# Kernel optimization log

Measured on AMD Instinct MI355X. Metric: run time of the kernel, lower is better.

The kernel has to match this reference:

```python
import jax, jax.numpy as jnp
import numpy as np

B, F_IN, N, S = 2, 128, 192, 192   # batch, in_features, n_nodes, seq (seq==n_nodes required by mask broadcast)
H, D = 4, 64                        # n_heads, n_hidden (out_features = H*D = 256)
NEG_SLOPE = 0.2


def setup_inputs() -> dict:
    key = jax.random.key(0)
    ks = jax.random.split(key, 6)
    X = jax.random.normal(ks[0], (B, F_IN, N, S), dtype=jnp.float32)
    A = jax.random.randint(ks[1], (N, N, 1), 0, 2, dtype=jnp.int32)
    W_lin = jax.random.normal(ks[2], (F_IN, H * D), dtype=jnp.float32) * 0.05
    b_lin = jax.random.uniform(ks[3], (H * D,), dtype=jnp.float32)
    W_attn = jax.random.normal(ks[4], (2 * D,), dtype=jnp.float32) * 0.05
    b_attn = jax.random.uniform(ks[5], (1,), dtype=jnp.float32)
    return {"X": X, "A": A, "W_lin": W_lin, "b_lin": b_lin,
            "W_attn": W_attn, "b_attn": b_attn}


def reference(X, A, W_lin, b_lin, W_attn, b_attn):
    # Dropout is identity (eval mode).
    b, f, n, s = X.shape
    x = jnp.transpose(X, (0, 3, 2, 1))                      # (b, s, n, f)
    g = (x @ W_lin + b_lin).reshape(b, s, n, H, D)          # (b, s, n, H, D)
    # attn is affine: attn(cat[g_i, g_j]) = a_src.g_i + a_dst.g_j + b_attn
    a_src, a_dst = W_attn[:D], W_attn[D:]
    s_src = jnp.einsum('bsnhd,d->bsnh', g, a_src)
    s_dst = jnp.einsum('bsnhd,d->bsnh', g, a_dst)
    e = s_src[:, :, :, None, :] + s_dst[:, :, None, :, :] + b_attn[0]  # (b, s, n_i, n_j, H)
    e = jnp.where(e >= 0, e, NEG_SLOPE * e)                 # LeakyReLU
    # torch masked_fill broadcast: mask (n,n,1,1) aligns with e dims (s, n_i, n_j, H)
    e = jnp.where(A[..., None] == 0, -jnp.inf, e)
    alphas = jax.nn.softmax(e, axis=1)                      # softmax over seq dim (dim=1, as in source)
    alphas = jnp.nan_to_num(alphas, nan=0.0)
    # einsum 'mnojh,klphf->mnohf': independent sums over j (alphas) and k,l,p (g)
    sum_g = g.sum(axis=(0, 1, 2))                           # (H, D)
    attn_res = alphas.sum(axis=3)[..., None] * sum_g        # (b, s, n, H, D)
    out = attn_res.reshape(b, s, n, H * D)                  # concat=True
    return jnp.transpose(out, (0, 3, 2, 1))                 # (b, out_features, n, s)
```

## Files before the change

kernel.cpp:

```cpp
#include <hip/hip_runtime.h>
#include <math.h>

#define B_ 2
#define F_ 128
#define N_ 192
#define S_ 192
#define NS_ (N_ * S_)
#define SLOPE 0.2f
#define LOG2E 1.4426950408889634f
#define NEG_INF (-__builtin_inff())

#if defined(__has_builtin)
#if __has_builtin(__builtin_amdgcn_exp2f)
#define EXP2(x) __builtin_amdgcn_exp2f(x)
#else
#define EXP2(x) exp2f(x)
#endif
#else
#define EXP2(x) exp2f(x)
#endif

__device__ __forceinline__ float lrelu(float e) { return fmaxf(e, SLOPE * e); }

#define OFF_WSRC 0
#define OFF_WDST 512
#define OFF_CSRC 1024
#define OFF_CDST 1028
#define OFF_SUMG 1040
#define OFF_PART 1296
#define OFF_SRC  2320
#define OFF_DST2 (OFF_SRC + 8 * NS_)
#define OFF_DST1 (OFF_DST2 + 8 * NS_)

__global__ __launch_bounds__(256) void kPre(const float* __restrict__ X,
                                            const float* __restrict__ W_lin,
                                            const float* __restrict__ b_lin,
                                            const float* __restrict__ W_attn,
                                            const float* __restrict__ b_attn,
                                            float* __restrict__ ws) {
    int blk = blockIdx.x, t = threadIdx.x;
    if (blk < 1024) {
        int sq = blk & 3, f = (blk >> 2) & 127, b = blk >> 9;
        const float4* p = (const float4*)(X + ((size_t)(b * F_ + f)) * NS_ + sq * 9216);
        float acc = 0.f;
#pragma unroll
        for (int k = 0; k < 9; k++) {
            float4 v = p[t + k * 256];
            acc += (v.x + v.y) + (v.z + v.w);
        }
        for (int o = 32; o; o >>= 1) acc += __shfl_down(acc, o, 64);
        __shared__ float red[4];
        if ((t & 63) == 0) red[t >> 6] = acc;
        __syncthreads();
        if (t == 0)
            ws[OFF_PART + sq * 256 + b * 128 + f] = (red[0] + red[1]) + (red[2] + red[3]);
    } else if (blk == 1024) {
        const float4* wa = (const float4*)W_attn;
        for (int c = t; c < 512; c += 256) {
            int f = c >> 2, h = c & 3;
            const float4* wl = (const float4*)(W_lin + f * 256 + h * 64);
            float as = 0.f, ad = 0.f;
#pragma unroll
            for (int q = 0; q < 16; q++) {
                float4 w = wl[q], a1 = wa[q], a2 = wa[16 + q];
                as += w.x * a1.x + w.y * a1.y + w.z * a1.z + w.w * a1.w;
                ad += w.x * a2.x + w.y * a2.y + w.z * a2.z + w.w * a2.w;
            }
            ws[OFF_WSRC + c] = as * LOG2E;
            ws[OFF_WDST + c] = ad * LOG2E;
        }
    } else {
        if (t < 4) {
            float c = 0.f;
            for (int d = 0; d < 64; d++) c += b_lin[t * 64 + d] * W_attn[d];
            ws[OFF_CSRC + t] = (c + b_attn[0]) * LOG2E;
        } else if (t < 8) {
            int h = t - 4;
            float c = 0.f;
            for (int d = 0; d < 64; d++) c += b_lin[h * 64 + d] * W_attn[64 + d];
            ws[OFF_CDST + h] = c * LOG2E;
        }
    }
}

__global__ __launch_bounds__(256) void kProj(const float* __restrict__ X,
                                             const int* __restrict__ A,
                                             const float* __restrict__ W_lin,
                                             const float* __restrict__ b_lin,
                                             float* __restrict__ ws) {
    __shared__ float4 wsl[128], wdl[128];
    __shared__ float red[4 * 64 * 9];
    __shared__ float xs[128];
    __shared__ float wbuf[4096];
    int t = threadIdx.x, blk = blockIdx.x;
    if (blk < 1152) {
        int n = blk % 192, bsc = blk / 192;
        int b = bsc / 3, sc = bsc % 3;
        if (t < 128) {
            wsl[t] = ((const float4*)(ws + OFF_WSRC))[t];
            wdl[t] = ((const float4*)(ws + OFF_WDST))[t];
        }
        __syncthreads();
        int fq = t >> 6, lane = t & 63;
        int s = sc * 64 + lane;
        float aS[4] = {0, 0, 0, 0}, aD[4] = {0, 0, 0, 0};
        const float* xp = X + (size_t)(b * F_) * NS_ + n * S_ + s;
        int f0 = fq * 32;
#pragma unroll 8
        for (int fi = 0; fi < 32; fi++) {
            float x = xp[(size_t)(f0 + fi) * NS_];
            float4 w1 = wsl[f0 + fi], w2 = wdl[f0 + fi];
            aS[0] += x * w1.x; aS[1] += x * w1.y; aS[2] += x * w1.z; aS[3] += x * w1.w;
            aD[0] += x * w2.x; aD[1] += x * w2.y; aD[2] += x * w2.z; aD[3] += x * w2.w;
        }
        float* rp = red + t * 9;
#pragma unroll
        for (int h = 0; h < 4; h++) { rp[h] = aS[h]; rp[4 + h] = aD[h]; }
        __syncthreads();
#pragma unroll
        for (int c = t; c < 512; c += 256) {
            int s_loc = c >> 3, k = c & 7;
            float v = red[s_loc * 9 + k] + red[(64 + s_loc) * 9 + k] +
                      red[(128 + s_loc) * 9 + k] + red[(192 + s_loc) * 9 + k];
            int ss = sc * 64 + s_loc;
            if (k < 4) {
                int bh = b * 4 + k;
                bool masked = (A[ss * 192 + n] == 0);
                ws[OFF_SRC + bh * NS_ + n * 192 + ss] =
                    masked ? NEG_INF : (v + ws[OFF_CSRC + k]);
            } else {
                int h = k - 4, bh = b * 4 + h;
                float dv = v + ws[OFF_CDST + h];
                ws[OFF_DST2 + bh * NS_ + n * 192 + ss] = dv;
                ws[OFF_DST1 + bh * NS_ + ss * 192 + n] = dv;
            }
        }
    } else {
        if (t < 128) {
            float v = 0.f;
#pragma unroll
            for (int q = 0; q < 8; q++) v += ws[OFF_PART + q * 128 + t];
            xs[t] = v;
        }
        float acc = 0.f;
        for (int ch = 0; ch < 8; ch++) {
            const float4* s4 = (const float4*)(W_lin + ch * 4096);
            __syncthreads();
#pragma unroll
            for (int k = 0; k < 4; k++) ((float4*)wbuf)[t + k * 256] = s4[t + k * 256];
            __syncthreads();
#pragma unroll
            for (int fi = 0; fi < 16; fi++) acc += xs[ch * 16 + fi] * wbuf[fi * 256 + t];
        }
        ws[OFF_SUMG + t] = acc + 73728.f * b_lin[t];
    }
}

__global__ __launch_bounds__(384) void kAttn(const float* __restrict__ ws,
                                             float* __restrict__ out) {
    int blk = blockIdx.x, t = threadIdx.x;
    int bh = blk & 7, iq = blk >> 3;
    int b = bh >> 2, h = bh & 3;
    __shared__ float p_sh[384];
    __shared__ float zpart[2 * 384];
    __shared__ float zr_sh[384];
    __shared__ float sg_sh[64];
    const float* src = ws + OFF_SRC + bh * NS_;
    const float* d1 = ws + OFF_DST1 + bh * NS_;
    const float* d2 = ws + OFF_DST2 + bh * NS_;
    if (t < 64) sg_sh[t] = ws[OFF_SUMG + h * 64 + t];
    p_sh[t] = src[iq * 384 + t];
    __syncthreads();

    {
        int sq = t / 192, j = t - sq * 192;
        float z0 = 0.f, z1 = 0.f;
        const float* d1p = d1 + j;
#pragma unroll 8
        for (int s = sq * 96; s < sq * 96 + 96; s++) {
            float q = d1p[s * 192];
            z0 += EXP2(lrelu(p_sh[s] + q));
            z1 += EXP2(lrelu(p_sh[192 + s] + q));
        }
        zpart[sq * 384 + j] = z0;
        zpart[sq * 384 + 192 + j] = z1;
    }
    __syncthreads();
    {
        float Z = zpart[t] + zpart[384 + t];
        zr_sh[t] = (Z != 0.f) ? (1.f / Z) : 0.f;
    }
    __syncthreads();

    {
        int i_loc = t / 192, s = t - i_loc * 192;
        float pv = p_sh[t];
        const float* zr = zr_sh + i_loc * 192;
        float acc = 0.f;
#pragma unroll 8
        for (int j = 0; j < 192; j++) {
            float q = d2[j * 192 + s];
            acc += EXP2(lrelu(pv + q)) * zr[j];
        }
        int i = iq * 2 + i_loc;
        float* op = out + (((size_t)(b * 256 + h * 64)) * 192 + i) * 192 + s;
#pragma unroll 8
        for (int d = 0; d < 64; d++)
            op[(size_t)d * NS_] = acc * sg_sh[d];
    }
}

extern "C" void kernel_launch(void* const* d_in, const int* in_sizes, int n_in,
                              void* d_out, int out_size, void* d_ws, size_t ws_size,
                              hipStream_t stream) {
    const float* X      = (const float*)d_in[0];
    const int*   A      = (const int*)d_in[1];
    const float* W_lin  = (const float*)d_in[2];
    const float* b_lin  = (const float*)d_in[3];
    const float* W_attn = (const float*)d_in[4];
    const float* b_attn = (const float*)d_in[5];
    float* out = (float*)d_out;
    float* ws  = (float*)d_ws;

    kPre<<<1026, 256, 0, stream>>>(X, W_lin, b_lin, W_attn, b_attn, ws);
    kProj<<<1153, 256, 0, stream>>>(X, A, W_lin, b_lin, ws);
    kAttn<<<768, 384, 0, stream>>>(ws, out);
}
```

Baseline: 150.9 us.

## Vectorize attention kernel loads and stores with float4 and split reductions

The attention kernel now has each thread handle four adjacent columns through float4 loads of the dst score arrays. It splits the seq and j reductions across more thread groups, combines the partial sums in shared memory, and writes the output with float4 stores spread over four d-quarters. The projection kernel's reduction index mapping is reordered so consecutive threads write consecutive s positions, which makes the global stores coalesced. This cuts per-thread memory instruction count and store traffic inefficiency, at the cost of extra shared-memory reduction passes and barriers.

```diff
diff --git a/kernel.cpp b/kernel.cpp
--- a/kernel.cpp
+++ b/kernel.cpp
@@ -119,7 +119,7 @@
         __syncthreads();
 #pragma unroll
         for (int c = t; c < 512; c += 256) {
-            int s_loc = c >> 3, k = c & 7;
+            int k = c >> 6, s_loc = c & 63;
             float v = red[s_loc * 9 + k] + red[(64 + s_loc) * 9 + k] +
                       red[(128 + s_loc) * 9 + k] + red[(192 + s_loc) * 9 + k];
             int ss = sc * 64 + s_loc;
@@ -162,8 +162,9 @@
     int bh = blk & 7, iq = blk >> 3;
     int b = bh >> 2, h = bh & 3;
     __shared__ float p_sh[384];
-    __shared__ float zpart[2 * 384];
+    __shared__ float zpart[16 * 192];
     __shared__ float zr_sh[384];
+    __shared__ float alpha_sh[384];
     __shared__ float sg_sh[64];
     const float* src = ws + OFF_SRC + bh * NS_;
     const float* d1 = ws + OFF_DST1 + bh * NS_;
@@ -173,40 +174,76 @@
     __syncthreads();
 
     {
-        int sq = t / 192, j = t - sq * 192;
-        float z0 = 0.f, z1 = 0.f;
-        const float* d1p = d1 + j;
-#pragma unroll 8
-        for (int s = sq * 96; s < sq * 96 + 96; s++) {
-            float q = d1p[s * 192];
-            z0 += EXP2(lrelu(p_sh[s] + q));
-            z1 += EXP2(lrelu(p_sh[192 + s] + q));
-        }
-        zpart[sq * 384 + j] = z0;
-        zpart[sq * 384 + 192 + j] = z1;
-    }
-    __syncthreads();
-    {
-        float Z = zpart[t] + zpart[384 + t];
-        zr_sh[t] = (Z != 0.f) ? (1.f / Z) : 0.f;
-    }
-    __syncthreads();
-
-    {
-        int i_loc = t / 192, s = t - i_loc * 192;
-        float pv = p_sh[t];
+        int sq = t / 48, j4 = t % 48;
+        float4 a0 = make_float4(0.f, 0.f, 0.f, 0.f);
+        float4 a1 = make_float4(0.f, 0.f, 0.f, 0.f);
+        const float* base = d1 + j4 * 4;
+        int s0 = sq * 24;
+#pragma unroll 4
+        for (int s = s0; s < s0 + 24; s++) {
+            float4 q = *(const float4*)(base + s * 192);
+            float p0 = p_sh[s], p1 = p_sh[192 + s];
+            a0.x += EXP2(lrelu(p0 + q.x)); a0.y += EXP2(lrelu(p0 + q.y));
+            a0.z += EXP2(lrelu(p0 + q.z)); a0.w += EXP2(lrelu(p0 + q.w));
+            a1.x += EXP2(lrelu(p1 + q.x)); a1.y += EXP2(lrelu(p1 + q.y));
+            a1.z += EXP2(lrelu(p1 + q.z)); a1.w += EXP2(lrelu(p1 + q.w));
+        }
+        *(float4*)&zpart[(sq * 2 + 0) * 192 + j4 * 4] = a0;
+        *(float4*)&zpart[(sq * 2 + 1) * 192 + j4 * 4] = a1;
+    }
+    __syncthreads();
+    {
+        int i_loc = t / 192, j = t % 192;
+        float Z = 0.f;
+#pragma unroll
+        for (int sq = 0; sq < 8; sq++) Z += zpart[(sq * 2 + i_loc) * 192 + j];
+        zr_sh[i_loc * 192 + j] = (Z != 0.f) ? (1.f / Z) : 0.f;
+    }
+    __syncthreads();
+
+    {
+        int jq = t / 96, rem = t % 96;
+        int i_loc = rem / 48, s4 = rem % 48;
+        float4 pv = *(const float4*)&p_sh[i_loc * 192 + s4 * 4];
         const float* zr = zr_sh + i_loc * 192;
-        float acc = 0.f;
-#pragma unroll 8
-        for (int j = 0; j < 192; j++) {
-            float q = d2[j * 192 + s];
-            acc += EXP2(lrelu(pv + q)) * zr[j];
-        }
+        const float* base = d2 + s4 * 4;
+        float4 acc = make_float4(0.f, 0.f, 0.f, 0.f);
+        int j0 = jq * 48;
+#pragma unroll 4
+        for (int j = j0; j < j0 + 48; j++) {
+            float4 q = *(const float4*)(base + j * 192);
+            float z = zr[j];
+            acc.x += EXP2(lrelu(pv.x + q.x)) * z;
+            acc.y += EXP2(lrelu(pv.y + q.y)) * z;
+            acc.z += EXP2(lrelu(pv.z + q.z)) * z;
+            acc.w += EXP2(lrelu(pv.w + q.w)) * z;
+        }
+        __syncthreads();
+        *(float4*)&zpart[((jq * 2 + i_loc) * 48 + s4) * 4] = acc;
+    }
+    __syncthreads();
+    {
+        int i_loc = t / 192, s = t % 192;
+        int s4 = s >> 2, c = s & 3;
+        float al = 0.f;
+#pragma unroll
+        for (int jq = 0; jq < 4; jq++) al += zpart[((jq * 2 + i_loc) * 48 + s4) * 4 + c];
+        alpha_sh[t] = al;
+    }
+    __syncthreads();
+
+    {
+        int dq = t / 96, rem = t % 96;
+        int i_loc = rem / 48, s4 = rem % 48;
+        float4 al = *(const float4*)&alpha_sh[i_loc * 192 + s4 * 4];
         int i = iq * 2 + i_loc;
-        float* op = out + (((size_t)(b * 256 + h * 64)) * 192 + i) * 192 + s;
-#pragma unroll 8
-        for (int d = 0; d < 64; d++)
-            op[(size_t)d * NS_] = acc * sg_sh[d];
+        float* op = out + (((size_t)(b * 256 + h * 64 + dq * 16)) * 192 + i) * 192 + s4 * 4;
+#pragma unroll 4
+        for (int d = 0; d < 16; d++) {
+            float g = sg_sh[dq * 16 + d];
+            float4 o = make_float4(al.x * g, al.y * g, al.z * g, al.w * g);
+            *(float4*)(op + (size_t)d * NS_) = o;
+        }
     }
 }
 
```

New measurement: 161.9 us. 7.3% more time.

## Split attention kernel into alpha compute and vectorized output broadcast kernel

Applied to the files above, without the earlier changes.

The attention kernel now writes the per-(b,h,i,s) alpha sums to workspace, and a new kernel broadcasts them against sum_g. That kernel writes the 75MB output with float4 stores, 16 feature rows per thread. This decouples the store-bound output phase from the exp-heavy alpha phase so the output writes can run at full bandwidth. It also reorders the projection scatter loop so consecutive threads write contiguous s positions. The cost is an extra kernel launch and a workspace round trip for alpha.

```diff
diff --git a/kernel.cpp b/kernel.cpp
--- a/kernel.cpp
+++ b/kernel.cpp
@@ -31,6 +31,7 @@
 #define OFF_SRC  2320
 #define OFF_DST2 (OFF_SRC + 8 * NS_)
 #define OFF_DST1 (OFF_DST2 + 8 * NS_)
+#define OFF_ALPHA (OFF_DST1 + 8 * NS_)
 
 __global__ __launch_bounds__(256) void kPre(const float* __restrict__ X,
                                             const float* __restrict__ W_lin,
@@ -119,7 +120,7 @@
         __syncthreads();
 #pragma unroll
         for (int c = t; c < 512; c += 256) {
-            int s_loc = c >> 3, k = c & 7;
+            int k = c >> 6, s_loc = c & 63;
             float v = red[s_loc * 9 + k] + red[(64 + s_loc) * 9 + k] +
                       red[(128 + s_loc) * 9 + k] + red[(192 + s_loc) * 9 + k];
             int ss = sc * 64 + s_loc;
@@ -156,19 +157,15 @@
     }
 }
 
-__global__ __launch_bounds__(384) void kAttn(const float* __restrict__ ws,
-                                             float* __restrict__ out) {
+__global__ __launch_bounds__(384) void kAlpha(float* __restrict__ ws) {
     int blk = blockIdx.x, t = threadIdx.x;
     int bh = blk & 7, iq = blk >> 3;
-    int b = bh >> 2, h = bh & 3;
     __shared__ float p_sh[384];
     __shared__ float zpart[2 * 384];
     __shared__ float zr_sh[384];
-    __shared__ float sg_sh[64];
     const float* src = ws + OFF_SRC + bh * NS_;
     const float* d1 = ws + OFF_DST1 + bh * NS_;
     const float* d2 = ws + OFF_DST2 + bh * NS_;
-    if (t < 64) sg_sh[t] = ws[OFF_SUMG + h * 64 + t];
     p_sh[t] = src[iq * 384 + t];
     __syncthreads();
 
@@ -203,10 +200,32 @@
             acc += EXP2(lrelu(pv + q)) * zr[j];
         }
         int i = iq * 2 + i_loc;
-        float* op = out + (((size_t)(b * 256 + h * 64)) * 192 + i) * 192 + s;
-#pragma unroll 8
-        for (int d = 0; d < 64; d++)
-            op[(size_t)d * NS_] = acc * sg_sh[d];
+        ws[OFF_ALPHA + bh * NS_ + i * 192 + s] = acc;
+    }
+}
+
+__global__ __launch_bounds__(256) void kOut(const float* __restrict__ ws,
+                                            float* __restrict__ out) {
+    __shared__ float sg[256];
+    int t = threadIdx.x;
+    sg[t] = ws[OFF_SUMG + t];
+    __syncthreads();
+    int v = blockIdx.x * 256 + t;
+    int s4 = v % 48;
+    int u = v / 48;
+    int i = u % 192; u /= 192;
+    int dq = u & 3;  u >>= 2;
+    int h = u & 3;
+    int b = u >> 2;
+    int bh = (b << 2) | h;
+    float4 al = *(const float4*)(ws + OFF_ALPHA + (bh * 192 + i) * 192 + s4 * 4);
+    float* op = out + (((size_t)(b * 256 + h * 64 + dq * 16)) * 192 + i) * 192 + s4 * 4;
+    const float* sgp = sg + h * 64 + dq * 16;
+#pragma unroll
+    for (int d = 0; d < 16; d++) {
+        float g = sgp[d];
+        float4 o = make_float4(al.x * g, al.y * g, al.z * g, al.w * g);
+        *(float4*)(op + (size_t)d * NS_) = o;
     }
 }
 
@@ -224,5 +243,6 @@
 
     kPre<<<1026, 256, 0, stream>>>(X, W_lin, b_lin, W_attn, b_attn, ws);
     kProj<<<1153, 256, 0, stream>>>(X, A, W_lin, b_lin, ws);
-    kAttn<<<768, 384, 0, stream>>>(ws, out);
-}
+    kAlpha<<<768, 384, 0, stream>>>(ws);
+    kOut<<<1152, 256, 0, stream>>>(ws, out);
+}
```

New measurement: 156.2 us. 3.5% more time.
